# Kernel optimization log

Measured on AMD Instinct MI355X. Metric: run time of the kernel, lower is better.

The kernel has to match this reference:

```python
import jax, jax.numpy as jnp
import numpy as np
from jax import lax

PRE_NMS_TOPN = 6000
POST_NMS_TOPN = 300
NMS_IOU = 0.7
VARIANCES = np.array([0.1, 0.1, 0.2, 0.2], dtype=np.float32)


def setup_inputs() -> dict:
    key = jax.random.key(0)
    k1, k2, k3, k4 = jax.random.split(key, 4)
    B, FH, FW, K = 32, 128, 128, 9
    A = FH * FW * K  # 147456 total anchors
    rpn_bbox_deltas = jax.random.normal(k1, (B, A, 4), dtype=jnp.float32) * 0.1
    rpn_labels = jax.random.normal(k2, (B, FH, FW, K), dtype=jnp.float32)
    # Anchors in [y1, x1, y2, x2] with y1<y2, x1<x2 on a ~1024px image.
    ctr = jax.random.uniform(k3, (A, 2), dtype=jnp.float32) * 1024.0
    wh = jax.random.uniform(k4, (A, 2), dtype=jnp.float32) * 224.0 + 32.0
    anchors = jnp.concatenate([ctr - 0.5 * wh, ctr + 0.5 * wh], axis=-1)
    return {"rpn_bbox_deltas": rpn_bbox_deltas, "rpn_labels": rpn_labels, "anchors": anchors}


def get_bboxes_from_deltas(anchors, deltas):
    # anchors: [A, 4] (y1,x1,y2,x2); deltas: [B, A, 4] (dy,dx,dh,dw)
    anc_w = anchors[..., 3] - anchors[..., 1]
    anc_h = anchors[..., 2] - anchors[..., 0]
    anc_cx = anchors[..., 1] + 0.5 * anc_w
    anc_cy = anchors[..., 0] + 0.5 * anc_h
    bb_w = jnp.exp(deltas[..., 3]) * anc_w
    bb_h = jnp.exp(deltas[..., 2]) * anc_h
    bb_cx = deltas[..., 1] * anc_w + anc_cx
    bb_cy = deltas[..., 0] * anc_h + anc_cy
    y1 = bb_cy - 0.5 * bb_h
    x1 = bb_cx - 0.5 * bb_w
    y2 = bb_h + y1
    x2 = bb_w + x1
    return jnp.stack([y1, x1, y2, x2], axis=-1)


def nms_per_image(boxes, scores, iou_threshold, num_keep):
    # boxes: [N, 4] sorted by descending score; scores: [N]
    y1, x1, y2, x2 = boxes[:, 0], boxes[:, 1], boxes[:, 2], boxes[:, 3]
    areas = (y2 - y1) * (x2 - x1)

    def step(scores_rem, _):
        idx = jnp.argmax(scores_rem)
        valid = jnp.isfinite(scores_rem[idx])
        b = boxes[idx]
        iy1 = jnp.maximum(b[0], y1)
        ix1 = jnp.maximum(b[1], x1)
        iy2 = jnp.minimum(b[2], y2)
        ix2 = jnp.minimum(b[3], x2)
        inter = jnp.clip(iy2 - iy1, 0.0) * jnp.clip(ix2 - ix1, 0.0)
        b_area = (b[2] - b[0]) * (b[3] - b[1])
        iou = inter / (areas + b_area - inter + 1e-9)
        # IoU(box, itself) == 1 > threshold, so the picked box is also suppressed.
        new_scores = jnp.where(iou > iou_threshold, -jnp.inf, scores_rem)
        return new_scores, (idx, valid)

    _, (keep_idx, valid) = lax.scan(step, scores, None, length=num_keep)
    vf = valid.astype(boxes.dtype)
    keep_boxes = boxes[keep_idx] * vf[:, None]  # zero-pad invalid slots
    keep_scores = scores[keep_idx] * vf
    return keep_boxes, keep_scores


def reference(rpn_bbox_deltas, rpn_labels, anchors):
    A = anchors.shape[0]
    B = rpn_bbox_deltas.shape[0]
    deltas = rpn_bbox_deltas.reshape(B, A, 4) * jnp.asarray(VARIANCES)
    labels = jax.nn.softmax(rpn_labels, axis=-1).reshape(B, A)
    rpn_bboxes = get_bboxes_from_deltas(anchors, deltas)  # [B, A, 4]
    # top-k pre-NMS filter (lax.top_k output is already sorted descending)
    pre_scores, pre_idx = lax.top_k(labels, PRE_NMS_TOPN)  # [B, P]
    pre_boxes = jnp.take_along_axis(rpn_bboxes, pre_idx[..., None], axis=1)  # [B, P, 4]
    nms_fn = lambda b, s: nms_per_image(b, s, NMS_IOU, POST_NMS_TOPN)
    roi_bboxes, roi_scores = jax.vmap(nms_fn)(pre_boxes, pre_scores)
    return roi_bboxes, roi_scores
```

## Files before the change

### kernel.cpp

```cpp
#include <hip/hip_runtime.h>
#include <cstdint>
#include <cstddef>

#pragma clang fp contract(off)

#define KCLS 9
#define PRE_N 6000
#define POST_N 300
#define NMS_IOU_T 0.7f
#define HIST_BLOCK 256
#define CHUNKS_PER_IMG 32
#define NMS_BLOCK 512
#define PICK_BLOCK 256
#define NSEG 4
#define SEG_CAP 4096

#define SUPP(pb, pa, mbx, mar, out) \
    bool out; { \
        float iy1_ = fmaxf((pb).x, (mbx).x); \
        float ix1_ = fmaxf((pb).y, (mbx).y); \
        float iy2_ = fminf((pb).z, (mbx).z); \
        float ix2_ = fminf((pb).w, (mbx).w); \
        float ih_ = iy2_ - iy1_; ih_ = ih_ > 0.f ? ih_ : 0.f; \
        float iw_ = ix2_ - ix1_; iw_ = iw_ > 0.f ? iw_ : 0.f; \
        float inter_ = ih_ * iw_; \
        float den_ = (mar) + (pa) - inter_ + 1e-9f; \
        float hi_ = 0.7000007f * den_; \
        float lo_ = 0.6999993f * den_; \
        out = inter_ > hi_; \
        if (inter_ >= lo_ && inter_ <= hi_) out = (inter_ / den_) > NMS_IOU_T; \
    }

__global__ void __launch_bounds__(256)
softmax_hist_kernel(const float* __restrict__ labels,
                    float* __restrict__ scores,
                    unsigned int* __restrict__ ghist,
                    int ngroups, int gpi) {
    __shared__ unsigned int h[2048];
    const int tid = threadIdx.x;
    for (int i = tid; i < 2048; i += 256) h[i] = 0u;
    __syncthreads();
    const int g = blockIdx.x * 256 + tid;
    if (g < ngroups) {
        const float* x = labels + (size_t)g * KCLS;
        float v[KCLS];
        float m = -1e30f;
        #pragma unroll
        for (int k = 0; k < KCLS; ++k) { v[k] = x[k]; m = fmaxf(m, v[k]); }
        float e[KCLS];
        float s = 0.f;
        #pragma unroll
        for (int k = 0; k < KCLS; ++k) { e[k] = expf(v[k] - m); s += e[k]; }
        float* o = scores + (size_t)g * KCLS;
        #pragma unroll
        for (int k = 0; k < KCLS; ++k) {
            float r = e[k] / s;
            o[k] = r;
            atomicAdd(&h[(__float_as_uint(r) >> 21) & 2047u], 1u);
        }
    }
    __syncthreads();
    const int img0 = (blockIdx.x * 256) / gpi;
    unsigned int* gh = ghist + (size_t)img0 * 2048;
    for (int i = tid; i < 2048; i += 256) {
        unsigned int c = h[i];
        if (c) atomicAdd(&gh[i], c);
    }
}

__global__ void hist_kernel(const float* __restrict__ scores,
                            unsigned int* __restrict__ ghist,
                            const unsigned int* __restrict__ state,
                            int A, int shift, int bins, unsigned int pmask) {
    __shared__ unsigned int h[2048];
    const int img = blockIdx.y;
    const int chunk = blockIdx.x;
    const int tid = threadIdx.x;
    for (int i = tid; i < bins; i += HIST_BLOCK) h[i] = 0u;
    __syncthreads();
    unsigned int prefix = pmask ? (state[img * 2 + 0] & pmask) : 0u;
    const int per = A / CHUNKS_PER_IMG;
    const float* sc = scores + (size_t)img * A + (size_t)chunk * per;
    for (int i = tid; i < per; i += HIST_BLOCK) {
        unsigned int v = __float_as_uint(sc[i]);
        if ((v & pmask) == prefix)
            atomicAdd(&h[(v >> shift) & (unsigned)(bins - 1)], 1u);
    }
    __syncthreads();
    unsigned int* gh = ghist + (size_t)img * 2048;
    for (int i = tid; i < bins; i += HIST_BLOCK) {
        unsigned int c = h[i];
        if (c) atomicAdd(&gh[i], c);
    }
}

__global__ void __launch_bounds__(PICK_BLOCK)
pick_kernel(const unsigned int* __restrict__ ghist,
            unsigned int* __restrict__ state,
            int shift, int bins, int first_pass) {
    const int img = blockIdx.x;
    const int t = threadIdx.x;
    const unsigned int* gh = ghist + (size_t)img * 2048;
    __shared__ unsigned int cnt[2048];
    __shared__ unsigned int ssum[PICK_BLOCK];
    const int per = bins / PICK_BLOCK;
    unsigned int my = 0;
    for (int i = 0; i < per; ++i) {
        unsigned int c = gh[t * per + i];
        cnt[t * per + i] = c;
        my += c;
    }
    ssum[t] = my;
    __syncthreads();
    for (int d = 1; d < PICK_BLOCK; d <<= 1) {
        unsigned int v = (t + d < PICK_BLOCK) ? ssum[t + d] : 0u;
        __syncthreads();
        ssum[t] += v;
        __syncthreads();
    }
    unsigned int prefix = first_pass ? 0u : state[img * 2 + 0];
    unsigned int krem = first_pass ? (unsigned)PRE_N : state[img * 2 + 1];
    unsigned int above = ssum[t] - my;
    if (above < krem && ssum[t] >= krem) {
        unsigned int cum = above;
        for (int b = per - 1; b >= 0; --b) {
            unsigned int c = cnt[t * per + b];
            if (cum + c >= krem) {
                state[img * 2 + 0] = prefix | ((unsigned int)(t * per + b) << shift);
                state[img * 2 + 1] = krem - cum;
                break;
            }
            cum += c;
        }
    }
}

#define CE(a, b, u) { if ((v[a] > v[b]) == (u)) { unsigned long long t_ = v[a]; v[a] = v[b]; v[b] = t_; } }
#define REG3(u) { CE(0,4,u) CE(1,5,u) CE(2,6,u) CE(3,7,u) \
                  CE(0,2,u) CE(1,3,u) CE(4,6,u) CE(5,7,u) \
                  CE(0,1,u) CE(2,3,u) CE(4,5,u) CE(6,7,u) }

__global__ void __launch_bounds__(512)
compact_sort_kernel(const float* __restrict__ scores,
                    const unsigned int* __restrict__ state,
                    unsigned long long* __restrict__ pool,
                    unsigned int* __restrict__ counts,
                    int A) {
    __shared__ unsigned long long lin[SEG_CAP];
    __shared__ unsigned int plo[2][SEG_CAP];
    __shared__ unsigned int phi[2][SEG_CAP];
    __shared__ unsigned int cnt;
    const int img = blockIdx.y;
    const int seg = blockIdx.x;
    const int tid = threadIdx.x;
    const int lane = tid & 63;
    const int w = tid >> 6;
    const float* sc = scores + (size_t)img * A;
    const unsigned int T = state[img * 2 + 0];

    if (tid == 0) cnt = 0u;
    for (int i = tid; i < SEG_CAP; i += 512) lin[i] = ~0ull;
    __syncthreads();

    const int ngr = A >> 6;
    const int nj = ngr / NSEG;
    for (int j = w; j < nj; j += 8) {
        int g = seg + j * NSEG;
        int i = (g << 6) + lane;
        unsigned int sv = __float_as_uint(sc[i]);
        bool push = (sv >= T);
        unsigned long long bal = __ballot(push ? 1 : 0);
        if (push) {
            int leader = __ffsll(bal) - 1;
            int rank = __popcll(bal & ((1ull << lane) - 1ull));
            unsigned int base = 0;
            if (lane == leader) base = atomicAdd(&cnt, (unsigned int)__popcll(bal));
            base = (unsigned int)__shfl((int)base, leader);
            unsigned int pos = base + (unsigned int)rank;
            if (pos < SEG_CAP)
                lin[pos] = (((unsigned long long)(~sv)) << 32) | (unsigned long long)(unsigned int)i;
        }
    }
    __syncthreads();

    int n = (int)cnt; if (n > SEG_CAP) n = SEG_CAP;
    int P2 = 512; while (P2 < n) P2 <<= 1;
    const int NT = P2 >> 3;
    const int t = tid;
    const bool act = (t < NT);

    unsigned long long v[8];
    if (act) {
        #pragma unroll
        for (int e = 0; e < 8; ++e) v[e] = lin[(t << 3) + e];
        CE(0,1,true) CE(2,3,false) CE(4,5,true) CE(6,7,false)
        CE(0,2,true) CE(1,3,true) CE(4,6,false) CE(5,7,false)
        CE(0,1,true) CE(2,3,true) CE(4,5,false) CE(6,7,false)
        bool u8 = ((t & 1) == 0);
        REG3(u8)
    }
    int b = 0;
    for (int k = 16; k <= P2; k <<= 1) {
        const bool up = (((t << 3) & k) == 0);
        for (int j = k >> 1; j >= 8; j >>= 1) {
            const int c = j >> 3;
            if (act) {
                #pragma unroll
                for (int e = 0; e < 8; ++e) {
                    int idx = e * NT + t;
                    plo[b][idx] = (unsigned int)v[e];
                    phi[b][idx] = (unsigned int)(v[e] >> 32);
                }
            }
            __syncthreads();
            if (act) {
                const int q = t ^ c;
                const bool keep_min = (up == ((t & c) == 0));
                #pragma unroll
                for (int e = 0; e < 8; ++e) {
                    int idx = e * NT + q;
                    unsigned long long wv = ((unsigned long long)phi[b][idx] << 32)
                                          | (unsigned long long)plo[b][idx];
                    bool less = v[e] < wv;
                    v[e] = (less == keep_min) ? v[e] : wv;
                }
            }
            b ^= 1;
        }
        if (act) { REG3(up) }
    }

    unsigned long long* gp = pool + ((size_t)img * NSEG + seg) * SEG_CAP;
    if (act) {
        #pragma unroll
        for (int e = 0; e < 8; ++e) {
            int r = (t << 3) + e;
            if (r < n) gp[r] = v[e];
        }
    }
    if (tid == 0) counts[img * NSEG + seg] = (unsigned int)n;
}

__global__ void __launch_bounds__(256)
rank_decode_kernel(const unsigned long long* __restrict__ pool,
                   const unsigned int* __restrict__ counts,
                   const float* __restrict__ deltas,
                   const float* __restrict__ anchors,
                   float* __restrict__ pre_boxes,
                   float* __restrict__ pre_scores,
                   int A) {
    __shared__ unsigned long long arr[2 * SEG_CAP];
    const int img = blockIdx.y;
    const int seg = blockIdx.x;
    const int tid = threadIdx.x;

    int c[NSEG], off[NSEG + 1];
    const unsigned long long* gp[NSEG];
    off[0] = 0;
    #pragma unroll
    for (int s = 0; s < NSEG; ++s) {
        int cs = (int)counts[img * NSEG + s];
        if (cs > SEG_CAP) cs = SEG_CAP;
        c[s] = cs;
        off[s + 1] = off[s] + cs;
        gp[s] = pool + ((size_t)img * NSEG + s) * SEG_CAP;
    }
    const int total = off[NSEG];
    const bool inlds = (total <= 2 * SEG_CAP);
    if (inlds) {
        #pragma unroll
        for (int s = 0; s < NSEG; ++s)
            for (int i = tid; i < c[s]; i += 256) arr[off[s] + i] = gp[s][i];
    }
    __syncthreads();

    const int m = c[seg];
    for (int i = tid; i < m; i += 256) {
        unsigned long long key = inlds ? arr[off[seg] + i] : gp[seg][i];
        int pos = i;
        #pragma unroll
        for (int s = 0; s < NSEG; ++s) {
            if (s == seg) continue;
            const unsigned long long* base = inlds ? (arr + off[s]) : gp[s];
            int lo = 0, hi = c[s];
            while (lo < hi) {
                int mid = (lo + hi) >> 1;
                if (base[mid] < key) lo = mid + 1; else hi = mid;
            }
            pos += lo;
        }
        if (pos < PRE_N) {
            unsigned int bidx = (unsigned int)(key & 0xFFFFFFFFull);
            unsigned int sbits = ~((unsigned int)(key >> 32));
            float score = __uint_as_float(sbits);
            float a0 = anchors[(size_t)bidx * 4 + 0];
            float a1 = anchors[(size_t)bidx * 4 + 1];
            float a2 = anchors[(size_t)bidx * 4 + 2];
            float a3 = anchors[(size_t)bidx * 4 + 3];
            const float* dd = deltas + ((size_t)img * A + bidx) * 4;
            float d0 = dd[0] * 0.1f;
            float d1 = dd[1] * 0.1f;
            float d2 = dd[2] * 0.2f;
            float d3 = dd[3] * 0.2f;
            float anc_w = a3 - a1;
            float anc_h = a2 - a0;
            float anc_cx = a1 + 0.5f * anc_w;
            float anc_cy = a0 + 0.5f * anc_h;
            float bb_w = expf(d3) * anc_w;
            float bb_h = expf(d2) * anc_h;
            float bb_cx = d1 * anc_w + anc_cx;
            float bb_cy = d0 * anc_h + anc_cy;
            float y1 = bb_cy - 0.5f * bb_h;
            float x1 = bb_cx - 0.5f * bb_w;
            float y2 = bb_h + y1;
            float x2 = bb_w + x1;
            float* ob = pre_boxes + ((size_t)img * PRE_N + pos) * 4;
            ob[0] = y1; ob[1] = x1; ob[2] = y2; ob[3] = x2;
            pre_scores[(size_t)img * PRE_N + pos] = score;
        }
    }
}

__global__ void __launch_bounds__(NMS_BLOCK)
nms_kernel(const float* __restrict__ pre_boxes,
           const float* __restrict__ pre_scores,
           float* __restrict__ out_boxes,
           float* __restrict__ out_scores) {
    const int img = blockIdx.x;
    const int tid = threadIdx.x;
    const int lane = tid & 63;
    const int grp = tid >> 6;
    const float4* bb4 = (const float4*)(pre_boxes + (size_t)img * PRE_N * 4);

    __shared__ float4 kept[POST_N];
    __shared__ float  kept_area[POST_N];
    __shared__ int    kept_idx[POST_N];
    __shared__ float4 chunkbox[64];
    __shared__ unsigned long long part[8][64];
    __shared__ unsigned long long supcol[64];
    __shared__ unsigned long long chunk_alive;
    __shared__ int kept_cnt;

    if (tid == 0) kept_cnt = 0;

    const int NCH = (PRE_N + 63) >> 6;

    float4 nb = make_float4(0.f, 0.f, 0.f, 0.f);
    if (grp == 0) nb = bb4[lane];

    for (int c = 0; c < NCH; ++c) {
        const int base = c << 6;
        if (grp == 0) chunkbox[lane] = nb;
        if (tid == 0) {
            int rem = PRE_N - base;
            chunk_alive = (rem >= 64) ? ~0ull : ((1ull << rem) - 1ull);
        }
        __syncthreads();

        if (grp == 0 && c + 1 < NCH) {
            int j = base + 64 + lane;
            nb = (j < PRE_N) ? bb4[j] : make_float4(0.f, 0.f, 0.f, 0.f);
        }

        const int K = kept_cnt;
        float4 mb = chunkbox[lane];
        float marea = (mb.z - mb.x) * (mb.w - mb.y);

        bool sup = false;
        for (int k = grp; k < K; k += 8) {
            float4 pb = kept[k];
            float pa = kept_area[k];
            SUPP(pb, pa, mb, marea, s)
            if (s) { sup = true; break; }
        }
        unsigned long long bal = __ballot(sup ? 1 : 0);
        if (lane == 0 && bal) atomicAnd(&chunk_alive, ~bal);

        unsigned long long pm = 0ull;
        #pragma unroll
        for (int u = 0; u < 8; ++u) {
            const int i = (grp << 3) + u;
            float4 pb = chunkbox[i];
            float pa = (pb.z - pb.x) * (pb.w - pb.y);
            SUPP(pb, pa, mb, marea, s)
            if (s) pm |= (1ull << i);
        }
        part[grp][lane] = pm;
        __syncthreads();

        if (grp == 0) {
            unsigned long long col = part[0][lane] | part[1][lane] | part[2][lane] | part[3][lane]
                                   | part[4][lane] | part[5][lane] | part[6][lane] | part[7][lane];
            supcol[lane] = col;
            const unsigned long long extm = chunk_alive;
            unsigned long long aliveset = 0ull;
            int kc = K;
            #pragma unroll 8
            for (int i = 0; i < 64; ++i) {
                unsigned long long mi = supcol[i];
                bool keep = (((extm >> i) & 1ull) != 0ull) &&
                            ((mi & aliveset) == 0ull) && (kc < POST_N);
                if (keep) {
                    if (lane == i) {
                        kept[kc] = mb;
                        kept_area[kc] = marea;
                        kept_idx[kc] = base + i;
                    }
                    aliveset |= (1ull << i);
                    ++kc;
                }
            }
            if (lane == 0) kept_cnt = kc;
        }
        __syncthreads();
        if (kept_cnt >= POST_N) break;
    }

    const int kc = kept_cnt;
    for (int r = tid; r < kc; r += NMS_BLOCK) {
        float4 bx = kept[r];
        float* ob = out_boxes + ((size_t)img * POST_N + r) * 4;
        ob[0] = bx.x; ob[1] = bx.y; ob[2] = bx.z; ob[3] = bx.w;
        out_scores[(size_t)img * POST_N + r] =
            pre_scores[(size_t)img * PRE_N + kept_idx[r]];
    }
}

extern "C" void kernel_launch(void* const* d_in, const int* in_sizes, int n_in,
                              void* d_out, int out_size, void* d_ws, size_t ws_size,
                              hipStream_t stream) {
    const float* deltas  = (const float*)d_in[0];
    const float* labels  = (const float*)d_in[1];
    const float* anchors = (const float*)d_in[2];
    float* out = (float*)d_out;

    const int A = in_sizes[2] / 4;
    const int B = in_sizes[0] / (A * 4);
    const int ngroups = in_sizes[1] / KCLS;
    const int gpi = ngroups / B;

    float* scores     = (float*)d_ws;
    float* pre_boxes  = scores + (size_t)B * A;
    float* pre_scores = pre_boxes + (size_t)B * PRE_N * 4;
    unsigned int* hist  = (unsigned int*)(pre_scores + (size_t)B * PRE_N);
    unsigned int* state = hist + (size_t)3 * B * 2048;
    unsigned long long* pool = (unsigned long long*)(state + (size_t)B * 2);
    unsigned int* counts = (unsigned int*)(pool + (size_t)B * NSEG * SEG_CAP);

    float* out_boxes  = out;
    float* out_scores = out + (size_t)B * POST_N * 4;

    hipMemsetAsync(d_out, 0, (size_t)out_size * sizeof(float), stream);
    hipMemsetAsync(hist, 0, (size_t)3 * B * 2048 * sizeof(unsigned int), stream);

    softmax_hist_kernel<<<(ngroups + 255) / 256, 256, 0, stream>>>(
        labels, scores, hist + (size_t)0 * B * 2048, ngroups, gpi);
    pick_kernel<<<B, PICK_BLOCK, 0, stream>>>(hist + (size_t)0 * B * 2048, state, 21, 2048, 1);

    dim3 hgrid(CHUNKS_PER_IMG, B);
    hist_kernel<<<hgrid, HIST_BLOCK, 0, stream>>>(scores, hist + (size_t)1 * B * 2048, state, A, 10, 2048, 0xFFE00000u);
    pick_kernel<<<B, PICK_BLOCK, 0, stream>>>(hist + (size_t)1 * B * 2048, state, 10, 2048, 0);
    hist_kernel<<<hgrid, HIST_BLOCK, 0, stream>>>(scores, hist + (size_t)2 * B * 2048, state, A, 0, 1024, 0xFFFFFC00u);
    pick_kernel<<<B, PICK_BLOCK, 0, stream>>>(hist + (size_t)2 * B * 2048, state, 0, 1024, 0);

    dim3 sgrid(NSEG, B);
    compact_sort_kernel<<<sgrid, 512, 0, stream>>>(scores, state, pool, counts, A);
    rank_decode_kernel<<<sgrid, 256, 0, stream>>>(pool, counts, deltas, anchors,
                                                  pre_boxes, pre_scores, A);

    nms_kernel<<<B, NMS_BLOCK, 0, stream>>>(pre_boxes, pre_scores, out_boxes, out_scores);
}
```

Baseline: 289.5 us.

## Fuse radix-select pick into histogram kernels via last-block pattern; widen sort segments

Removes the three separate pick_kernel launches by having the last block per image (detected with an atomic done counter and threadfences) run the prefix-scan pick inline at the end of each histogram kernel. This cuts kernel launch count and the serialization gaps between small launches. It also changes the compact/sort segmentation from 4 segments of 4096 to 8 segments of 2048, and enlarges the rank kernel's LDS buffer to match, which spreads sort work over more blocks. The risks are reliance on the memory fences for correctness and more binary searches per key in the rank merge.

```diff
diff --git a/kernel.cpp b/kernel.cpp
--- a/kernel.cpp
+++ b/kernel.cpp
@@ -11,9 +11,9 @@
 #define HIST_BLOCK 256
 #define CHUNKS_PER_IMG 32
 #define NMS_BLOCK 512
-#define PICK_BLOCK 256
-#define NSEG 4
-#define SEG_CAP 4096
+#define NSEG 8
+#define SEG_CAP 2048
+#define RANK_LDS 8192
 
 #define SUPP(pb, pa, mbx, mar, out) \
     bool out; { \
@@ -31,12 +31,54 @@
         if (inter_ >= lo_ && inter_ <= hi_) out = (inter_ / den_) > NMS_IOU_T; \
     }
 
+__device__ __forceinline__ void pick_inline(
+        const unsigned int* __restrict__ gh, unsigned int* __restrict__ state_img,
+        int shift, int bins, int first_pass,
+        unsigned int* cnt , unsigned int* ssum ) {
+    const int t = threadIdx.x;
+    const int per = bins >> 8;
+    unsigned int my = 0;
+    for (int i = 0; i < per; ++i) {
+        unsigned int c = __hip_atomic_load(&gh[t * per + i],
+                                           __ATOMIC_RELAXED, __HIP_MEMORY_SCOPE_AGENT);
+        cnt[t * per + i] = c;
+        my += c;
+    }
+    ssum[t] = my;
+    __syncthreads();
+    for (int d = 1; d < 256; d <<= 1) {
+        unsigned int v = (t + d < 256) ? ssum[t + d] : 0u;
+        __syncthreads();
+        ssum[t] += v;
+        __syncthreads();
+    }
+    unsigned int prefix = first_pass ? 0u : state_img[0];
+    unsigned int krem = first_pass ? (unsigned)PRE_N : state_img[1];
+    unsigned int above = ssum[t] - my;
+    if (above < krem && ssum[t] >= krem) {
+        unsigned int cum = above;
+        for (int b = per - 1; b >= 0; --b) {
+            unsigned int c = cnt[t * per + b];
+            if (cum + c >= krem) {
+                state_img[0] = prefix | ((unsigned int)(t * per + b) << shift);
+                state_img[1] = krem - cum;
+                break;
+            }
+            cum += c;
+        }
+    }
+}
+
 __global__ void __launch_bounds__(256)
 softmax_hist_kernel(const float* __restrict__ labels,
                     float* __restrict__ scores,
                     unsigned int* __restrict__ ghist,
-                    int ngroups, int gpi) {
+                    unsigned int* __restrict__ state,
+                    unsigned int* __restrict__ done,
+                    int ngroups, int bpi) {
     __shared__ unsigned int h[2048];
+    __shared__ unsigned int ssum[256];
+    __shared__ int lastblk;
     const int tid = threadIdx.x;
     for (int i = tid; i < 2048; i += 256) h[i] = 0u;
     __syncthreads();
@@ -60,25 +102,40 @@
         }
     }
     __syncthreads();
-    const int img0 = (blockIdx.x * 256) / gpi;
-    unsigned int* gh = ghist + (size_t)img0 * 2048;
+    const int img = blockIdx.x / bpi;
+    unsigned int* gh = ghist + (size_t)img * 2048;
     for (int i = tid; i < 2048; i += 256) {
         unsigned int c = h[i];
         if (c) atomicAdd(&gh[i], c);
     }
-}
-
-__global__ void hist_kernel(const float* __restrict__ scores,
-                            unsigned int* __restrict__ ghist,
-                            const unsigned int* __restrict__ state,
-                            int A, int shift, int bins, unsigned int pmask) {
+    __syncthreads();
+    if (tid == 0) {
+        __threadfence();
+        unsigned int d = atomicAdd(&done[img], 1u);
+        lastblk = (d == (unsigned)(bpi - 1));
+    }
+    __syncthreads();
+    if (lastblk) {
+        __threadfence();
+        pick_inline(gh, state + (size_t)img * 2, 21, 2048, 1, h, ssum);
+    }
+}
+
+__global__ void __launch_bounds__(HIST_BLOCK)
+hist_pick_kernel(const float* __restrict__ scores,
+                 unsigned int* __restrict__ ghist,
+                 unsigned int* __restrict__ state,
+                 unsigned int* __restrict__ done,
+                 int A, int shift, int bins, unsigned int pmask) {
     __shared__ unsigned int h[2048];
+    __shared__ unsigned int ssum[256];
+    __shared__ int lastblk;
     const int img = blockIdx.y;
     const int chunk = blockIdx.x;
     const int tid = threadIdx.x;
     for (int i = tid; i < bins; i += HIST_BLOCK) h[i] = 0u;
     __syncthreads();
-    unsigned int prefix = pmask ? (state[img * 2 + 0] & pmask) : 0u;
+    unsigned int prefix = state[img * 2 + 0] & pmask;
     const int per = A / CHUNKS_PER_IMG;
     const float* sc = scores + (size_t)img * A + (size_t)chunk * per;
     for (int i = tid; i < per; i += HIST_BLOCK) {
@@ -92,46 +149,16 @@
         unsigned int c = h[i];
         if (c) atomicAdd(&gh[i], c);
     }
-}
-
-__global__ void __launch_bounds__(PICK_BLOCK)
-pick_kernel(const unsigned int* __restrict__ ghist,
-            unsigned int* __restrict__ state,
-            int shift, int bins, int first_pass) {
-    const int img = blockIdx.x;
-    const int t = threadIdx.x;
-    const unsigned int* gh = ghist + (size_t)img * 2048;
-    __shared__ unsigned int cnt[2048];
-    __shared__ unsigned int ssum[PICK_BLOCK];
-    const int per = bins / PICK_BLOCK;
-    unsigned int my = 0;
-    for (int i = 0; i < per; ++i) {
-        unsigned int c = gh[t * per + i];
-        cnt[t * per + i] = c;
-        my += c;
-    }
-    ssum[t] = my;
-    __syncthreads();
-    for (int d = 1; d < PICK_BLOCK; d <<= 1) {
-        unsigned int v = (t + d < PICK_BLOCK) ? ssum[t + d] : 0u;
-        __syncthreads();
-        ssum[t] += v;
-        __syncthreads();
-    }
-    unsigned int prefix = first_pass ? 0u : state[img * 2 + 0];
-    unsigned int krem = first_pass ? (unsigned)PRE_N : state[img * 2 + 1];
-    unsigned int above = ssum[t] - my;
-    if (above < krem && ssum[t] >= krem) {
-        unsigned int cum = above;
-        for (int b = per - 1; b >= 0; --b) {
-            unsigned int c = cnt[t * per + b];
-            if (cum + c >= krem) {
-                state[img * 2 + 0] = prefix | ((unsigned int)(t * per + b) << shift);
-                state[img * 2 + 1] = krem - cum;
-                break;
-            }
-            cum += c;
-        }
+    __syncthreads();
+    if (tid == 0) {
+        __threadfence();
+        unsigned int d = atomicAdd(&done[img], 1u);
+        lastblk = (d == (unsigned)(CHUNKS_PER_IMG - 1));
+    }
+    __syncthreads();
+    if (lastblk) {
+        __threadfence();
+        pick_inline(gh, state + (size_t)img * 2, shift, bins, 0, h, ssum);
     }
 }
 
@@ -249,7 +276,7 @@
                    float* __restrict__ pre_boxes,
                    float* __restrict__ pre_scores,
                    int A) {
-    __shared__ unsigned long long arr[2 * SEG_CAP];
+    __shared__ unsigned long long arr[RANK_LDS];
     const int img = blockIdx.y;
     const int seg = blockIdx.x;
     const int tid = threadIdx.x;
@@ -266,7 +293,7 @@
         gp[s] = pool + ((size_t)img * NSEG + s) * SEG_CAP;
     }
     const int total = off[NSEG];
-    const bool inlds = (total <= 2 * SEG_CAP);
+    const bool inlds = (total <= RANK_LDS);
     if (inlds) {
         #pragma unroll
         for (int s = 0; s < NSEG; ++s)
@@ -438,12 +465,14 @@
     const int B = in_sizes[0] / (A * 4);
     const int ngroups = in_sizes[1] / KCLS;
     const int gpi = ngroups / B;
+    const int bpi = gpi / 256;
 
     float* scores     = (float*)d_ws;
     float* pre_boxes  = scores + (size_t)B * A;
     float* pre_scores = pre_boxes + (size_t)B * PRE_N * 4;
     unsigned int* hist  = (unsigned int*)(pre_scores + (size_t)B * PRE_N);
-    unsigned int* state = hist + (size_t)3 * B * 2048;
+    unsigned int* done  = hist + (size_t)3 * B * 2048;
+    unsigned int* state = done + (size_t)3 * B;
     unsigned long long* pool = (unsigned long long*)(state + (size_t)B * 2);
     unsigned int* counts = (unsigned int*)(pool + (size_t)B * NSEG * SEG_CAP);
 
@@ -451,17 +480,16 @@
     float* out_scores = out + (size_t)B * POST_N * 4;
 
     hipMemsetAsync(d_out, 0, (size_t)out_size * sizeof(float), stream);
-    hipMemsetAsync(hist, 0, (size_t)3 * B * 2048 * sizeof(unsigned int), stream);
+    hipMemsetAsync(hist, 0, ((size_t)3 * B * 2048 + 3 * B + 2 * B) * sizeof(unsigned int), stream);
 
     softmax_hist_kernel<<<(ngroups + 255) / 256, 256, 0, stream>>>(
-        labels, scores, hist + (size_t)0 * B * 2048, ngroups, gpi);
-    pick_kernel<<<B, PICK_BLOCK, 0, stream>>>(hist + (size_t)0 * B * 2048, state, 21, 2048, 1);
+        labels, scores, hist + (size_t)0 * B * 2048, state, done + 0 * B, ngroups, bpi);
 
     dim3 hgrid(CHUNKS_PER_IMG, B);
-    hist_kernel<<<hgrid, HIST_BLOCK, 0, stream>>>(scores, hist + (size_t)1 * B * 2048, state, A, 10, 2048, 0xFFE00000u);
-    pick_kernel<<<B, PICK_BLOCK, 0, stream>>>(hist + (size_t)1 * B * 2048, state, 10, 2048, 0);
-    hist_kernel<<<hgrid, HIST_BLOCK, 0, stream>>>(scores, hist + (size_t)2 * B * 2048, state, A, 0, 1024, 0xFFFFFC00u);
-    pick_kernel<<<B, PICK_BLOCK, 0, stream>>>(hist + (size_t)2 * B * 2048, state, 0, 1024, 0);
+    hist_pick_kernel<<<hgrid, HIST_BLOCK, 0, stream>>>(
+        scores, hist + (size_t)1 * B * 2048, state, done + 1 * B, A, 10, 2048, 0xFFE00000u);
+    hist_pick_kernel<<<hgrid, HIST_BLOCK, 0, stream>>>(
+        scores, hist + (size_t)2 * B * 2048, state, done + 2 * B, A, 0, 1024, 0xFFFFFC00u);
 
     dim3 sgrid(NSEG, B);
     compact_sort_kernel<<<sgrid, 512, 0, stream>>>(scores, state, pool, counts, A);
```

Result: slower. 403.2 us (+39.3%).
